# Kernel tuning notes

Measured on AMD Instinct MI355X. Metric: run time of the kernel, lower is better.

The kernel has to match this reference:

```python
import jax, jax.numpy as jnp
import numpy as np

N = 100_000  # nodes
E = 1_600_000  # edges (before self-loops)
NEG_SLOPE = 0.2  # PyG GATConv default leaky_relu slope


def gat_layer(x, W, a_src, a_dst, b, src, dst, heads, out_ch, concat):
    # x: [N, Fin]; W: [Fin, heads*out_ch]; a_src/a_dst: [1, heads, out_ch]
    h = (x @ W).reshape(-1, heads, out_ch)            # [N, H, C]
    alpha_s = jnp.sum(h * a_src, axis=-1)             # [N, H]
    alpha_d = jnp.sum(h * a_dst, axis=-1)             # [N, H]
    e = jax.nn.leaky_relu(alpha_s[src] + alpha_d[dst], NEG_SLOPE)  # [E', H]
    # softmax over edges grouped by destination node (self-loops guarantee
    # every node has at least one incoming edge)
    m = jax.ops.segment_max(e, dst, num_segments=N)   # [N, H]
    p = jnp.exp(e - m[dst])                           # [E', H]
    s = jax.ops.segment_sum(p, dst, num_segments=N)   # [N, H]
    alpha = p / s[dst]                                # [E', H]
    out = jax.ops.segment_sum(alpha[:, :, None] * h[src], dst, num_segments=N)  # [N,H,C]
    out = out.reshape(-1, heads * out_ch) if concat else out.mean(axis=1)
    return out + b


def setup_inputs() -> dict:
    key = jax.random.key(0)
    ks = jax.random.split(key, 8)

    def glorot(k, shape):
        return (jax.random.normal(k, shape, jnp.float32) / np.sqrt(np.float32(shape[0]))).astype(jnp.float32)

    x = jax.random.normal(ks[0], (N, 512), jnp.float32)
    edge_index = jax.random.randint(ks[1], (2, E), 0, N, dtype=jnp.int64)
    W1 = glorot(ks[2], (512, 64))
    att_src1 = jax.random.normal(ks[3], (1, 8, 8), jnp.float32) * 0.1
    att_dst1 = jax.random.normal(ks[4], (1, 8, 8), jnp.float32) * 0.1
    b1 = jnp.zeros((64,), jnp.float32)
    W2 = glorot(ks[5], (64, 128))
    att_src2 = jax.random.normal(ks[6], (1, 1, 128), jnp.float32) * 0.1
    att_dst2 = jax.random.normal(ks[7], (1, 1, 128), jnp.float32) * 0.1
    b2 = jnp.zeros((128,), jnp.float32)
    return {"x": x, "edge_index": edge_index, "W1": W1, "att_src1": att_src1,
            "att_dst1": att_dst1, "b1": b1, "W2": W2, "att_src2": att_src2,
            "att_dst2": att_dst2, "b2": b2}


def reference(x, edge_index, W1, att_src1, att_dst1, b1, W2, att_src2, att_dst2, b2):
    # PyG GATConv adds self-loops by default
    loop = jnp.arange(N, dtype=edge_index.dtype)
    src = jnp.concatenate([edge_index[0], loop])
    dst = jnp.concatenate([edge_index[1], loop])
    h = gat_layer(x, W1, att_src1, att_dst1, b1, src, dst, heads=8, out_ch=8, concat=True)
    h = jax.nn.elu(h)
    z = gat_layer(h, W2, att_src2, att_dst2, b2, src, dst, heads=1, out_ch=128, concat=False)
    return z
```

## Files before the change

kernel.cpp:

```cpp
#include <hip/hip_runtime.h>
#include <math.h>

#define NNODES 100000

__device__ __forceinline__ float lrelu(float v) { return v > 0.f ? v : 0.2f * v; }

#define SWZ(row) ((((row) & 3) ^ (((row) >> 3) & 7)) << 2)

__global__ __launch_bounds__(128) void gemm1_k(const float* __restrict__ x,
                                               const float* __restrict__ W,
                                               float* __restrict__ h1, int Nn) {
    __shared__ float xs[128][64];
    __shared__ float ws[64][64];
    int r0 = blockIdx.x * 128;
    int t = threadIdx.x;
    int ty = t >> 3, tx = t & 7;
    float acc0[8][4] = {};
    float acc1[8][4] = {};
    for (int kb = 0; kb < 512; kb += 64) {
        for (int l = t; l < 2048; l += 128) {
            int row = l >> 4;
            int c4 = (l & 15) << 2;
            int gr = r0 + row;
            float4 v = make_float4(0.f, 0.f, 0.f, 0.f);
            if (gr < Nn) v = *reinterpret_cast<const float4*>(&x[(size_t)gr * 512 + kb + c4]);
            *reinterpret_cast<float4*>(&xs[row][c4 ^ SWZ(row)]) = v;
        }
        for (int l = t; l < 1024; l += 128) {
            int row = l >> 4;
            int c4 = (l & 15) << 2;
            *reinterpret_cast<float4*>(&ws[row][c4]) =
                *reinterpret_cast<const float4*>(&W[(size_t)(kb + row) * 64 + c4]);
        }
        __syncthreads();
#pragma unroll 1
        for (int k0 = 0; k0 < 64; k0 += 4) {
            float4 av[8];
#pragma unroll
            for (int i = 0; i < 8; ++i) {
                int row = ty * 8 + i;
                av[i] = *reinterpret_cast<const float4*>(&xs[row][k0 ^ SWZ(row)]);
            }
            float4 b0[4], b1[4];
#pragma unroll
            for (int kk = 0; kk < 4; ++kk) {
                b0[kk] = *reinterpret_cast<const float4*>(&ws[k0 + kk][tx * 4]);
                b1[kk] = *reinterpret_cast<const float4*>(&ws[k0 + kk][32 + tx * 4]);
            }
#pragma unroll
            for (int kk = 0; kk < 4; ++kk) {
#pragma unroll
                for (int i = 0; i < 8; ++i) {
                    float a = (kk == 0) ? av[i].x : (kk == 1) ? av[i].y : (kk == 2) ? av[i].z : av[i].w;
                    acc0[i][0] += a * b0[kk].x; acc0[i][1] += a * b0[kk].y;
                    acc0[i][2] += a * b0[kk].z; acc0[i][3] += a * b0[kk].w;
                    acc1[i][0] += a * b1[kk].x; acc1[i][1] += a * b1[kk].y;
                    acc1[i][2] += a * b1[kk].z; acc1[i][3] += a * b1[kk].w;
                }
            }
        }
        __syncthreads();
    }
#pragma unroll
    for (int i = 0; i < 8; ++i) {
        int gr = r0 + ty * 8 + i;
        if (gr < Nn) {
            *reinterpret_cast<float4*>(&h1[(size_t)gr * 64 + tx * 4]) =
                make_float4(acc0[i][0], acc0[i][1], acc0[i][2], acc0[i][3]);
            *reinterpret_cast<float4*>(&h1[(size_t)gr * 64 + 32 + tx * 4]) =
                make_float4(acc1[i][0], acc1[i][1], acc1[i][2], acc1[i][3]);
        }
    }
}

__global__ __launch_bounds__(256) void gemm2_k(const float* __restrict__ xin,
                                               const float* __restrict__ W,
                                               float* __restrict__ h2, int Nn) {
    __shared__ float xs[128][64];
    __shared__ float ws[64][128];
    int r0 = blockIdx.x * 128;
    int t = threadIdx.x;
    int ty = t >> 4, tx = t & 15;
    for (int l = t; l < 2048; l += 256) {
        int row = l >> 4;
        int c4 = (l & 15) << 2;
        int gr = r0 + row;
        float4 v = make_float4(0.f, 0.f, 0.f, 0.f);
        if (gr < Nn) v = *reinterpret_cast<const float4*>(&xin[(size_t)gr * 64 + c4]);
        *reinterpret_cast<float4*>(&xs[row][c4 ^ SWZ(row)]) = v;
    }
    for (int l = t; l < 2048; l += 256) {
        int row = l >> 5;
        int c4 = (l & 31) << 2;
        *reinterpret_cast<float4*>(&ws[row][c4]) =
            *reinterpret_cast<const float4*>(&W[(size_t)row * 128 + c4]);
    }
    __syncthreads();
    float acc0[8][4] = {};
    float acc1[8][4] = {};
#pragma unroll 1
    for (int k0 = 0; k0 < 64; k0 += 4) {
        float4 av[8];
#pragma unroll
        for (int i = 0; i < 8; ++i) {
            int row = ty * 8 + i;
            av[i] = *reinterpret_cast<const float4*>(&xs[row][k0 ^ SWZ(row)]);
        }
        float4 b0[4], b1[4];
#pragma unroll
        for (int kk = 0; kk < 4; ++kk) {
            b0[kk] = *reinterpret_cast<const float4*>(&ws[k0 + kk][tx * 4]);
            b1[kk] = *reinterpret_cast<const float4*>(&ws[k0 + kk][64 + tx * 4]);
        }
#pragma unroll
        for (int kk = 0; kk < 4; ++kk) {
#pragma unroll
            for (int i = 0; i < 8; ++i) {
                float a = (kk == 0) ? av[i].x : (kk == 1) ? av[i].y : (kk == 2) ? av[i].z : av[i].w;
                acc0[i][0] += a * b0[kk].x; acc0[i][1] += a * b0[kk].y;
                acc0[i][2] += a * b0[kk].z; acc0[i][3] += a * b0[kk].w;
                acc1[i][0] += a * b1[kk].x; acc1[i][1] += a * b1[kk].y;
                acc1[i][2] += a * b1[kk].z; acc1[i][3] += a * b1[kk].w;
            }
        }
    }
#pragma unroll
    for (int i = 0; i < 8; ++i) {
        int gr = r0 + ty * 8 + i;
        if (gr < Nn) {
            *reinterpret_cast<float4*>(&h2[(size_t)gr * 128 + tx * 4]) =
                make_float4(acc0[i][0], acc0[i][1], acc0[i][2], acc0[i][3]);
            *reinterpret_cast<float4*>(&h2[(size_t)gr * 128 + 64 + tx * 4]) =
                make_float4(acc1[i][0], acc1[i][1], acc1[i][2], acc1[i][3]);
        }
    }
}

__global__ __launch_bounds__(256) void attn1_k(const float* __restrict__ h1,
                                               const float* __restrict__ asrc,
                                               const float* __restrict__ adst,
                                               float* __restrict__ as1,
                                               float* __restrict__ ad1, int Nn) {
    int t = blockIdx.x * 256 + threadIdx.x;
    int n = t >> 3, h = t & 7;
    if (n >= Nn) return;
    const float* hp = h1 + (size_t)n * 64 + h * 8;
    float s = 0.f, d = 0.f;
#pragma unroll
    for (int c = 0; c < 8; ++c) {
        float v = hp[c];
        s += v * asrc[h * 8 + c];
        d += v * adst[h * 8 + c];
    }
    as1[(size_t)n * 8 + h] = s;
    ad1[(size_t)n * 8 + h] = d;
}

__global__ __launch_bounds__(256) void attn2_k(const float* __restrict__ h2,
                                               const float* __restrict__ asrc,
                                               const float* __restrict__ adst,
                                               float* __restrict__ as2,
                                               float* __restrict__ ad2, int Nn) {
    int wid = threadIdx.x >> 6, lane = threadIdx.x & 63;
    int n = blockIdx.x * 4 + wid;
    if (n >= Nn) return;
    float v0 = h2[(size_t)n * 128 + lane];
    float v1 = h2[(size_t)n * 128 + 64 + lane];
    float s = v0 * asrc[lane] + v1 * asrc[64 + lane];
    float d = v0 * adst[lane] + v1 * adst[64 + lane];
#pragma unroll
    for (int off = 32; off >= 1; off >>= 1) {
        s += __shfl_xor(s, off);
        d += __shfl_xor(d, off);
    }
    if (lane == 0) { as2[n] = s; ad2[n] = d; }
}

__global__ __launch_bounds__(256) void hist_k(const int* __restrict__ ei, int E, int Etot,
                                              int* __restrict__ indeg) {
    int e = blockIdx.x * 256 + threadIdx.x;
    if (e >= Etot) return;
    int d = (e < E) ? ei[E + e] : (e - E);
    atomicAdd(&indeg[d], 1);
}

__global__ __launch_bounds__(256) void scanA_k(const int* __restrict__ indeg,
                                               int* __restrict__ indptr,
                                               int* __restrict__ bsums, int Nn) {
    __shared__ int sd[256];
    int t = threadIdx.x;
    int i0 = blockIdx.x * 2048 + t * 8;
    int v[8], ex[8];
    int run = 0;
#pragma unroll
    for (int j = 0; j < 8; ++j) {
        int i = i0 + j;
        v[j] = (i < Nn) ? indeg[i] : 0;
        ex[j] = run;
        run += v[j];
    }
    sd[t] = run;
    __syncthreads();
    for (int off = 1; off < 256; off <<= 1) {
        int a = (t >= off) ? sd[t - off] : 0;
        __syncthreads();
        sd[t] += a;
        __syncthreads();
    }
    int texc = sd[t] - run;
#pragma unroll
    for (int j = 0; j < 8; ++j) {
        int i = i0 + j;
        if (i < Nn) indptr[i] = texc + ex[j];
    }
    if (t == 0) bsums[blockIdx.x] = sd[255];
}

__global__ void scanB_k(int* __restrict__ bsums, int nb) {
    if (threadIdx.x == 0 && blockIdx.x == 0) {
        int run = 0;
        for (int b = 0; b < nb; ++b) {
            int x = bsums[b];
            bsums[b] = run;
            run += x;
        }
    }
}

__global__ __launch_bounds__(256) void scanC_k(int* __restrict__ indptr,
                                               const int* __restrict__ bsums,
                                               int* __restrict__ cursor, int Nn, int Etot) {
    int t = threadIdx.x;
    int b = blockIdx.x;
    int base = bsums[b];
    int i0 = b * 2048 + t * 8;
#pragma unroll
    for (int j = 0; j < 8; ++j) {
        int i = i0 + j;
        if (i < Nn) {
            int val = indptr[i] + base;
            indptr[i] = val;
            cursor[i] = val;
        }
    }
    if (b == 0 && t == 0) indptr[Nn] = Etot;
}

__global__ __launch_bounds__(256) void fill_k(const int* __restrict__ ei, int E, int Etot,
                                              int* __restrict__ cursor, int* __restrict__ col) {
    int e = blockIdx.x * 256 + threadIdx.x;
    if (e >= Etot) return;
    int s, d;
    if (e < E) { s = ei[e]; d = ei[E + e]; }
    else { s = e - E; d = e - E; }
    int pos = atomicAdd(&cursor[d], 1);
    col[pos] = s;
}

__global__ __launch_bounds__(256) void agg1_k(const float* __restrict__ h1,
                                              const float* __restrict__ as1,
                                              const float* __restrict__ ad1,
                                              const int* __restrict__ indptr,
                                              const int* __restrict__ col,
                                              const float* __restrict__ b1,
                                              float* __restrict__ h1a, int Nn) {
    int wid = threadIdx.x >> 6, lane = threadIdx.x & 63;
    int n = blockIdx.x * 4 + wid;
    if (n >= Nn) return;
    int beg = indptr[n], end = indptr[n + 1];
    int h = lane & 7, eo = lane >> 3;
    float adn = ad1[(size_t)n * 8 + h];
    float ss = 0.f;
    for (int i = beg + eo; i < end; i += 8) {
        int s = col[i];
        ss += __expf(lrelu(as1[(size_t)s * 8 + h] + adn));
    }
    ss += __shfl_xor(ss, 8);
    ss += __shfl_xor(ss, 16);
    ss += __shfl_xor(ss, 32);
    int hb = lane >> 3;
    float sb = __shfl(ss, hb);
    float ab = __shfl(adn, hb);
    float inv = 1.f / sb;
    const float* __restrict__ h1l = h1 + lane;
    float acc0 = 0.f, acc1 = 0.f, acc2 = 0.f, acc3 = 0.f;
    float acc4 = 0.f, acc5 = 0.f, acc6 = 0.f, acc7 = 0.f;
    int i = beg;
    for (; i + 8 <= end; i += 8) {
        int s0 = col[i], s1 = col[i + 1], s2 = col[i + 2], s3 = col[i + 3];
        int s4 = col[i + 4], s5 = col[i + 5], s6 = col[i + 6], s7 = col[i + 7];
        float w0 = __expf(lrelu(as1[(size_t)s0 * 8 + hb] + ab));
        float w1 = __expf(lrelu(as1[(size_t)s1 * 8 + hb] + ab));
        float w2 = __expf(lrelu(as1[(size_t)s2 * 8 + hb] + ab));
        float w3 = __expf(lrelu(as1[(size_t)s3 * 8 + hb] + ab));
        float w4 = __expf(lrelu(as1[(size_t)s4 * 8 + hb] + ab));
        float w5 = __expf(lrelu(as1[(size_t)s5 * 8 + hb] + ab));
        float w6 = __expf(lrelu(as1[(size_t)s6 * 8 + hb] + ab));
        float w7 = __expf(lrelu(as1[(size_t)s7 * 8 + hb] + ab));
        acc0 += w0 * h1l[(size_t)s0 * 64];
        acc1 += w1 * h1l[(size_t)s1 * 64];
        acc2 += w2 * h1l[(size_t)s2 * 64];
        acc3 += w3 * h1l[(size_t)s3 * 64];
        acc4 += w4 * h1l[(size_t)s4 * 64];
        acc5 += w5 * h1l[(size_t)s5 * 64];
        acc6 += w6 * h1l[(size_t)s6 * 64];
        acc7 += w7 * h1l[(size_t)s7 * 64];
    }
    for (; i < end; ++i) {
        int s = col[i];
        acc0 += __expf(lrelu(as1[(size_t)s * 8 + hb] + ab)) * h1l[(size_t)s * 64];
    }
    float o = (((acc0 + acc1) + (acc2 + acc3)) + ((acc4 + acc5) + (acc6 + acc7))) * inv + b1[lane];
    h1a[(size_t)n * 64 + lane] = o > 0.f ? o : expm1f(o);
}

__global__ __launch_bounds__(256) void agg2_k(const float* __restrict__ h2,
                                              const float* __restrict__ as2,
                                              const float* __restrict__ ad2,
                                              const int* __restrict__ indptr,
                                              const int* __restrict__ col,
                                              const float* __restrict__ b2,
                                              float* __restrict__ out, int Nn) {
    int wid = threadIdx.x >> 6, lane = threadIdx.x & 63;
    int n = blockIdx.x * 4 + wid;
    if (n >= Nn) return;
    int beg = indptr[n], end = indptr[n + 1];
    float adn = ad2[n];
    float ss = 0.f;
    for (int i = beg + lane; i < end; i += 64) {
        ss += __expf(lrelu(as2[col[i]] + adn));
    }
#pragma unroll
    for (int off = 32; off >= 1; off >>= 1) ss += __shfl_xor(ss, off);
    float inv = 1.f / ss;
    const float* __restrict__ h2l = h2 + lane;
    float a00 = 0.f, a01 = 0.f, a02 = 0.f, a03 = 0.f;
    float a04 = 0.f, a05 = 0.f, a06 = 0.f, a07 = 0.f;
    float a10 = 0.f, a11 = 0.f, a12 = 0.f, a13 = 0.f;
    float a14 = 0.f, a15 = 0.f, a16 = 0.f, a17 = 0.f;
    int i = beg;
    for (; i + 8 <= end; i += 8) {
        int s0 = col[i], s1 = col[i + 1], s2 = col[i + 2], s3 = col[i + 3];
        int s4 = col[i + 4], s5 = col[i + 5], s6 = col[i + 6], s7 = col[i + 7];
        float w0 = __expf(lrelu(as2[s0] + adn));
        float w1 = __expf(lrelu(as2[s1] + adn));
        float w2 = __expf(lrelu(as2[s2] + adn));
        float w3 = __expf(lrelu(as2[s3] + adn));
        float w4 = __expf(lrelu(as2[s4] + adn));
        float w5 = __expf(lrelu(as2[s5] + adn));
        float w6 = __expf(lrelu(as2[s6] + adn));
        float w7 = __expf(lrelu(as2[s7] + adn));
        a00 += w0 * h2l[(size_t)s0 * 128]; a10 += w0 * h2l[(size_t)s0 * 128 + 64];
        a01 += w1 * h2l[(size_t)s1 * 128]; a11 += w1 * h2l[(size_t)s1 * 128 + 64];
        a02 += w2 * h2l[(size_t)s2 * 128]; a12 += w2 * h2l[(size_t)s2 * 128 + 64];
        a03 += w3 * h2l[(size_t)s3 * 128]; a13 += w3 * h2l[(size_t)s3 * 128 + 64];
        a04 += w4 * h2l[(size_t)s4 * 128]; a14 += w4 * h2l[(size_t)s4 * 128 + 64];
        a05 += w5 * h2l[(size_t)s5 * 128]; a15 += w5 * h2l[(size_t)s5 * 128 + 64];
        a06 += w6 * h2l[(size_t)s6 * 128]; a16 += w6 * h2l[(size_t)s6 * 128 + 64];
        a07 += w7 * h2l[(size_t)s7 * 128]; a17 += w7 * h2l[(size_t)s7 * 128 + 64];
    }
    for (; i < end; ++i) {
        int s = col[i];
        float w = __expf(lrelu(as2[s] + adn));
        a00 += w * h2l[(size_t)s * 128];
        a10 += w * h2l[(size_t)s * 128 + 64];
    }
    float r0 = ((a00 + a01) + (a02 + a03)) + ((a04 + a05) + (a06 + a07));
    float r1 = ((a10 + a11) + (a12 + a13)) + ((a14 + a15) + (a16 + a17));
    out[(size_t)n * 128 + lane] = r0 * inv + b2[lane];
    out[(size_t)n * 128 + 64 + lane] = r1 * inv + b2[64 + lane];
}

extern "C" void kernel_launch(void* const* d_in, const int* in_sizes, int n_in,
                              void* d_out, int out_size, void* d_ws, size_t ws_size,
                              hipStream_t stream) {
    const float* x = (const float*)d_in[0];
    const int* ei = (const int*)d_in[1];
    const float* W1 = (const float*)d_in[2];
    const float* asrc1 = (const float*)d_in[3];
    const float* adst1 = (const float*)d_in[4];
    const float* b1 = (const float*)d_in[5];
    const float* W2 = (const float*)d_in[6];
    const float* asrc2 = (const float*)d_in[7];
    const float* adst2 = (const float*)d_in[8];
    const float* b2 = (const float*)d_in[9];
    float* out = (float*)d_out;

    const int Nn = NNODES;
    const int E = in_sizes[1] / 2;
    const int Etot = E + Nn;

    char* w = (char*)d_ws;
    auto alloc = [&](size_t bytes) {
        char* p = w;
        w += (bytes + 255) & ~(size_t)255;
        return p;
    };
    float* h1 = (float*)alloc((size_t)Nn * 64 * 4);
    float* h1a = (float*)alloc((size_t)Nn * 64 * 4);
    float* h2 = (float*)alloc((size_t)Nn * 128 * 4);
    float* as1 = (float*)alloc((size_t)Nn * 8 * 4);
    float* ad1 = (float*)alloc((size_t)Nn * 8 * 4);
    float* as2 = (float*)alloc((size_t)Nn * 4);
    float* ad2 = (float*)alloc((size_t)Nn * 4);
    int* indeg = (int*)alloc((size_t)(Nn + 1) * 4);
    int* indptr = (int*)alloc((size_t)(Nn + 1) * 4);
    int* cursor = (int*)alloc((size_t)Nn * 4);
    int* bsums = (int*)alloc(4096);
    int* col = (int*)alloc((size_t)Etot * 4);

    const int NBLK = (Nn + 2047) / 2048;

    hipMemsetAsync(indeg, 0, (size_t)Nn * 4, stream);
    gemm1_k<<<(Nn + 127) / 128, 128, 0, stream>>>(x, W1, h1, Nn);
    attn1_k<<<(Nn * 8 + 255) / 256, 256, 0, stream>>>(h1, asrc1, adst1, as1, ad1, Nn);
    hist_k<<<(Etot + 255) / 256, 256, 0, stream>>>(ei, E, Etot, indeg);
    scanA_k<<<NBLK, 256, 0, stream>>>(indeg, indptr, bsums, Nn);
    scanB_k<<<1, 64, 0, stream>>>(bsums, NBLK);
    scanC_k<<<NBLK, 256, 0, stream>>>(indptr, bsums, cursor, Nn, Etot);
    fill_k<<<(Etot + 255) / 256, 256, 0, stream>>>(ei, E, Etot, cursor, col);
    agg1_k<<<(Nn + 3) / 4, 256, 0, stream>>>(h1, as1, ad1, indptr, col, b1, h1a, Nn);
    gemm2_k<<<(Nn + 127) / 128, 256, 0, stream>>>(h1a, W2, h2, Nn);
    attn2_k<<<(Nn + 3) / 4, 256, 0, stream>>>(h2, asrc2, adst2, as2, ad2, Nn);
    agg2_k<<<(Nn + 3) / 4, 256, 0, stream>>>(h2, as2, ad2, indptr, col, b2, out, Nn);
}
```

Before: 1.010 ms.

## Prefetch next K-tile into registers in gemm1 and enlarge block to 256 rows

After: 883.0 us. -12.6%, faster.

```diff
diff --git a/kernel.cpp b/kernel.cpp
--- a/kernel.cpp
+++ b/kernel.cpp
@@ -7,56 +7,101 @@
 
 #define SWZ(row) ((((row) & 3) ^ (((row) >> 3) & 7)) << 2)
 
-__global__ __launch_bounds__(128) void gemm1_k(const float* __restrict__ x,
+__global__ __launch_bounds__(256) void gemm1_k(const float* __restrict__ x,
                                                const float* __restrict__ W,
                                                float* __restrict__ h1, int Nn) {
-    __shared__ float xs[128][64];
+    __shared__ float xs[256][64];
     __shared__ float ws[64][64];
-    int r0 = blockIdx.x * 128;
+    int r0 = blockIdx.x * 256;
     int t = threadIdx.x;
     int ty = t >> 3, tx = t & 7;
-    float acc0[8][4] = {};
-    float acc1[8][4] = {};
+    float4 xr[16], wr[4];
+    float acc[8][8] = {};
+
+#pragma unroll
+    for (int n = 0; n < 16; ++n) {
+        int l = t + n * 256;
+        int row = l >> 4, c4 = (l & 15) << 2;
+        int gr = r0 + row;
+        xr[n] = make_float4(0.f, 0.f, 0.f, 0.f);
+        if (gr < Nn) xr[n] = *reinterpret_cast<const float4*>(&x[(size_t)gr * 512 + c4]);
+    }
+#pragma unroll
+    for (int n = 0; n < 4; ++n) {
+        int l = t + n * 256;
+        int row = l >> 4, c4 = (l & 15) << 2;
+        wr[n] = *reinterpret_cast<const float4*>(&W[(size_t)row * 64 + c4]);
+    }
+#pragma unroll
+    for (int n = 0; n < 16; ++n) {
+        int l = t + n * 256;
+        int row = l >> 4, c4 = (l & 15) << 2;
+        *reinterpret_cast<float4*>(&xs[row][c4 ^ SWZ(row)]) = xr[n];
+    }
+#pragma unroll
+    for (int n = 0; n < 4; ++n) {
+        int l = t + n * 256;
+        int row = l >> 4, c4 = (l & 15) << 2;
+        *reinterpret_cast<float4*>(&ws[row][c4]) = wr[n];
+    }
+    __syncthreads();
+
     for (int kb = 0; kb < 512; kb += 64) {
-        for (int l = t; l < 2048; l += 128) {
-            int row = l >> 4;
-            int c4 = (l & 15) << 2;
-            int gr = r0 + row;
-            float4 v = make_float4(0.f, 0.f, 0.f, 0.f);
-            if (gr < Nn) v = *reinterpret_cast<const float4*>(&x[(size_t)gr * 512 + kb + c4]);
-            *reinterpret_cast<float4*>(&xs[row][c4 ^ SWZ(row)]) = v;
-        }
-        for (int l = t; l < 1024; l += 128) {
-            int row = l >> 4;
-            int c4 = (l & 15) << 2;
-            *reinterpret_cast<float4*>(&ws[row][c4]) =
-                *reinterpret_cast<const float4*>(&W[(size_t)(kb + row) * 64 + c4]);
-        }
-        __syncthreads();
+        bool more = (kb + 64 < 512);
+        if (more) {
+#pragma unroll
+            for (int n = 0; n < 16; ++n) {
+                int l = t + n * 256;
+                int row = l >> 4, c4 = (l & 15) << 2;
+                int gr = r0 + row;
+                xr[n] = make_float4(0.f, 0.f, 0.f, 0.f);
+                if (gr < Nn) xr[n] = *reinterpret_cast<const float4*>(&x[(size_t)gr * 512 + kb + 64 + c4]);
+            }
+#pragma unroll
+            for (int n = 0; n < 4; ++n) {
+                int l = t + n * 256;
+                int row = l >> 4, c4 = (l & 15) << 2;
+                wr[n] = *reinterpret_cast<const float4*>(&W[(size_t)(kb + 64 + row) * 64 + c4]);
+            }
+        }
 #pragma unroll 1
         for (int k0 = 0; k0 < 64; k0 += 4) {
-            float4 av[8];
+            float4 av[8], ba[4], bb[4];
 #pragma unroll
             for (int i = 0; i < 8; ++i) {
                 int row = ty * 8 + i;
                 av[i] = *reinterpret_cast<const float4*>(&xs[row][k0 ^ SWZ(row)]);
             }
-            float4 b0[4], b1[4];
 #pragma unroll
             for (int kk = 0; kk < 4; ++kk) {
-                b0[kk] = *reinterpret_cast<const float4*>(&ws[k0 + kk][tx * 4]);
-                b1[kk] = *reinterpret_cast<const float4*>(&ws[k0 + kk][32 + tx * 4]);
+                ba[kk] = *reinterpret_cast<const float4*>(&ws[k0 + kk][tx * 8]);
+                bb[kk] = *reinterpret_cast<const float4*>(&ws[k0 + kk][tx * 8 + 4]);
             }
 #pragma unroll
             for (int kk = 0; kk < 4; ++kk) {
 #pragma unroll
                 for (int i = 0; i < 8; ++i) {
                     float a = (kk == 0) ? av[i].x : (kk == 1) ? av[i].y : (kk == 2) ? av[i].z : av[i].w;
-                    acc0[i][0] += a * b0[kk].x; acc0[i][1] += a * b0[kk].y;
-                    acc0[i][2] += a * b0[kk].z; acc0[i][3] += a * b0[kk].w;
-                    acc1[i][0] += a * b1[kk].x; acc1[i][1] += a * b1[kk].y;
-                    acc1[i][2] += a * b1[kk].z; acc1[i][3] += a * b1[kk].w;
+                    acc[i][0] += a * ba[kk].x; acc[i][1] += a * ba[kk].y;
+                    acc[i][2] += a * ba[kk].z; acc[i][3] += a * ba[kk].w;
+                    acc[i][4] += a * bb[kk].x; acc[i][5] += a * bb[kk].y;
+                    acc[i][6] += a * bb[kk].z; acc[i][7] += a * bb[kk].w;
                 }
+            }
+        }
+        __syncthreads();
+        if (more) {
+#pragma unroll
+            for (int n = 0; n < 16; ++n) {
+                int l = t + n * 256;
+                int row = l >> 4, c4 = (l & 15) << 2;
+                *reinterpret_cast<float4*>(&xs[row][c4 ^ SWZ(row)]) = xr[n];
+            }
+#pragma unroll
+            for (int n = 0; n < 4; ++n) {
+                int l = t + n * 256;
+                int row = l >> 4, c4 = (l & 15) << 2;
+                *reinterpret_cast<float4*>(&ws[row][c4]) = wr[n];
             }
         }
         __syncthreads();
@@ -65,10 +110,10 @@
     for (int i = 0; i < 8; ++i) {
         int gr = r0 + ty * 8 + i;
         if (gr < Nn) {
-            *reinterpret_cast<float4*>(&h1[(size_t)gr * 64 + tx * 4]) =
-                make_float4(acc0[i][0], acc0[i][1], acc0[i][2], acc0[i][3]);
-            *reinterpret_cast<float4*>(&h1[(size_t)gr * 64 + 32 + tx * 4]) =
-                make_float4(acc1[i][0], acc1[i][1], acc1[i][2], acc1[i][3]);
+            *reinterpret_cast<float4*>(&h1[(size_t)gr * 64 + tx * 8]) =
+                make_float4(acc[i][0], acc[i][1], acc[i][2], acc[i][3]);
+            *reinterpret_cast<float4*>(&h1[(size_t)gr * 64 + tx * 8 + 4]) =
+                make_float4(acc[i][4], acc[i][5], acc[i][6], acc[i][7]);
         }
     }
 }
@@ -82,16 +127,14 @@
     int t = threadIdx.x;
     int ty = t >> 4, tx = t & 15;
     for (int l = t; l < 2048; l += 256) {
-        int row = l >> 4;
-        int c4 = (l & 15) << 2;
+        int row = l >> 4, c4 = (l & 15) << 2;
         int gr = r0 + row;
         float4 v = make_float4(0.f, 0.f, 0.f, 0.f);
         if (gr < Nn) v = *reinterpret_cast<const float4*>(&xin[(size_t)gr * 64 + c4]);
         *reinterpret_cast<float4*>(&xs[row][c4 ^ SWZ(row)]) = v;
     }
     for (int l = t; l < 2048; l += 256) {
-        int row = l >> 5;
-        int c4 = (l & 31) << 2;
+        int row = l >> 5, c4 = (l & 31) << 2;
         *reinterpret_cast<float4*>(&ws[row][c4]) =
             *reinterpret_cast<const float4*>(&W[(size_t)row * 128 + c4]);
     }
@@ -100,27 +143,26 @@
     float acc1[8][4] = {};
 #pragma unroll 1
     for (int k0 = 0; k0 < 64; k0 += 4) {
-        float4 av[8];
+        float4 av[8], ba[4], bb[4];
 #pragma unroll
         for (int i = 0; i < 8; ++i) {
             int row = ty * 8 + i;
             av[i] = *reinterpret_cast<const float4*>(&xs[row][k0 ^ SWZ(row)]);
         }
-        float4 b0[4], b1[4];
 #pragma unroll
         for (int kk = 0; kk < 4; ++kk) {
-            b0[kk] = *reinterpret_cast<const float4*>(&ws[k0 + kk][tx * 4]);
-            b1[kk] = *reinterpret_cast<const float4*>(&ws[k0 + kk][64 + tx * 4]);
+            ba[kk] = *reinterpret_cast<const float4*>(&ws[k0 + kk][tx * 4]);
+            bb[kk] = *reinterpret_cast<const float4*>(&ws[k0 + kk][64 + tx * 4]);
         }
 #pragma unroll
         for (int kk = 0; kk < 4; ++kk) {
 #pragma unroll
             for (int i = 0; i < 8; ++i) {
                 float a = (kk == 0) ? av[i].x : (kk == 1) ? av[i].y : (kk == 2) ? av[i].z : av[i].w;
-                acc0[i][0] += a * b0[kk].x; acc0[i][1] += a * b0[kk].y;
-                acc0[i][2] += a * b0[kk].z; acc0[i][3] += a * b0[kk].w;
-                acc1[i][0] += a * b1[kk].x; acc1[i][1] += a * b1[kk].y;
-                acc1[i][2] += a * b1[kk].z; acc1[i][3] += a * b1[kk].w;
+                acc0[i][0] += a * ba[kk].x; acc0[i][1] += a * ba[kk].y;
+                acc0[i][2] += a * ba[kk].z; acc0[i][3] += a * ba[kk].w;
+                acc1[i][0] += a * bb[kk].x; acc1[i][1] += a * bb[kk].y;
+                acc1[i][2] += a * bb[kk].z; acc1[i][3] += a * bb[kk].w;
             }
         }
     }
@@ -412,7 +454,7 @@
     const int NBLK = (Nn + 2047) / 2048;
 
     hipMemsetAsync(indeg, 0, (size_t)Nn * 4, stream);
-    gemm1_k<<<(Nn + 127) / 128, 128, 0, stream>>>(x, W1, h1, Nn);
+    gemm1_k<<<(Nn + 255) / 256, 256, 0, stream>>>(x, W1, h1, Nn);
     attn1_k<<<(Nn * 8 + 255) / 256, 256, 0, stream>>>(h1, asrc1, adst1, as1, ad1, Nn);
     hist_k<<<(Etot + 255) / 256, 256, 0, stream>>>(ei, E, Etot, indeg);
     scanA_k<<<NBLK, 256, 0, stream>>>(indeg, indptr, bsums, Nn);
```

## Read GEMM weights directly from global memory and retile threads in both GEMMs

Applied to the files above, without the earlier changes.

New measurement: 944.5 us. -6.5%, faster.

```diff
diff --git a/kernel.cpp b/kernel.cpp
--- a/kernel.cpp
+++ b/kernel.cpp
@@ -7,68 +7,59 @@
 
 #define SWZ(row) ((((row) & 3) ^ (((row) >> 3) & 7)) << 2)
 
-__global__ __launch_bounds__(128) void gemm1_k(const float* __restrict__ x,
+__global__ __launch_bounds__(256) void gemm1_k(const float* __restrict__ x,
                                                const float* __restrict__ W,
                                                float* __restrict__ h1, int Nn) {
     __shared__ float xs[128][64];
-    __shared__ float ws[64][64];
     int r0 = blockIdx.x * 128;
     int t = threadIdx.x;
     int ty = t >> 3, tx = t & 7;
-    float acc0[8][4] = {};
-    float acc1[8][4] = {};
+    int srow = t >> 4;
+    int sc4 = (t & 15) << 2;
+    float acc[4][8] = {};
     for (int kb = 0; kb < 512; kb += 64) {
-        for (int l = t; l < 2048; l += 128) {
-            int row = l >> 4;
-            int c4 = (l & 15) << 2;
+        __syncthreads();
+#pragma unroll
+        for (int n = 0; n < 8; ++n) {
+            int row = srow + n * 16;
             int gr = r0 + row;
-            float4 v = make_float4(0.f, 0.f, 0.f, 0.f);
-            if (gr < Nn) v = *reinterpret_cast<const float4*>(&x[(size_t)gr * 512 + kb + c4]);
-            *reinterpret_cast<float4*>(&xs[row][c4 ^ SWZ(row)]) = v;
-        }
-        for (int l = t; l < 1024; l += 128) {
-            int row = l >> 4;
-            int c4 = (l & 15) << 2;
-            *reinterpret_cast<float4*>(&ws[row][c4]) =
-                *reinterpret_cast<const float4*>(&W[(size_t)(kb + row) * 64 + c4]);
+            int cr = gr < Nn ? gr : Nn - 1;
+            float4 v = *reinterpret_cast<const float4*>(&x[(size_t)cr * 512 + kb + sc4]);
+            *reinterpret_cast<float4*>(&xs[row][sc4 ^ SWZ(row)]) = v;
         }
         __syncthreads();
+        const float* Wb = W + (size_t)kb * 64;
 #pragma unroll 1
         for (int k0 = 0; k0 < 64; k0 += 4) {
-            float4 av[8];
-#pragma unroll
-            for (int i = 0; i < 8; ++i) {
-                int row = ty * 8 + i;
+            float4 av[4];
+#pragma unroll
+            for (int i = 0; i < 4; ++i) {
+                int row = ty * 4 + i;
                 av[i] = *reinterpret_cast<const float4*>(&xs[row][k0 ^ SWZ(row)]);
             }
-            float4 b0[4], b1[4];
 #pragma unroll
             for (int kk = 0; kk < 4; ++kk) {
-                b0[kk] = *reinterpret_cast<const float4*>(&ws[k0 + kk][tx * 4]);
-                b1[kk] = *reinterpret_cast<const float4*>(&ws[k0 + kk][32 + tx * 4]);
-            }
-#pragma unroll
-            for (int kk = 0; kk < 4; ++kk) {
-#pragma unroll
-                for (int i = 0; i < 8; ++i) {
+                float4 b0 = *reinterpret_cast<const float4*>(&Wb[(k0 + kk) * 64 + tx * 8]);
+                float4 b1 = *reinterpret_cast<const float4*>(&Wb[(k0 + kk) * 64 + tx * 8 + 4]);
+#pragma unroll
+                for (int i = 0; i < 4; ++i) {
                     float a = (kk == 0) ? av[i].x : (kk == 1) ? av[i].y : (kk == 2) ? av[i].z : av[i].w;
-                    acc0[i][0] += a * b0[kk].x; acc0[i][1] += a * b0[kk].y;
-                    acc0[i][2] += a * b0[kk].z; acc0[i][3] += a * b0[kk].w;
-                    acc1[i][0] += a * b1[kk].x; acc1[i][1] += a * b1[kk].y;
-                    acc1[i][2] += a * b1[kk].z; acc1[i][3] += a * b1[kk].w;
+                    acc[i][0] += a * b0.x; acc[i][1] += a * b0.y;
+                    acc[i][2] += a * b0.z; acc[i][3] += a * b0.w;
+                    acc[i][4] += a * b1.x; acc[i][5] += a * b1.y;
+                    acc[i][6] += a * b1.z; acc[i][7] += a * b1.w;
                 }
             }
         }
-        __syncthreads();
-    }
-#pragma unroll
-    for (int i = 0; i < 8; ++i) {
-        int gr = r0 + ty * 8 + i;
+    }
+#pragma unroll
+    for (int i = 0; i < 4; ++i) {
+        int gr = r0 + ty * 4 + i;
         if (gr < Nn) {
-            *reinterpret_cast<float4*>(&h1[(size_t)gr * 64 + tx * 4]) =
-                make_float4(acc0[i][0], acc0[i][1], acc0[i][2], acc0[i][3]);
-            *reinterpret_cast<float4*>(&h1[(size_t)gr * 64 + 32 + tx * 4]) =
-                make_float4(acc1[i][0], acc1[i][1], acc1[i][2], acc1[i][3]);
+            *reinterpret_cast<float4*>(&h1[(size_t)gr * 64 + tx * 8]) =
+                make_float4(acc[i][0], acc[i][1], acc[i][2], acc[i][3]);
+            *reinterpret_cast<float4*>(&h1[(size_t)gr * 64 + tx * 8 + 4]) =
+                make_float4(acc[i][4], acc[i][5], acc[i][6], acc[i][7]);
         }
     }
 }
@@ -77,61 +68,59 @@
                                                const float* __restrict__ W,
                                                float* __restrict__ h2, int Nn) {
     __shared__ float xs[128][64];
-    __shared__ float ws[64][128];
     int r0 = blockIdx.x * 128;
     int t = threadIdx.x;
-    int ty = t >> 4, tx = t & 15;
-    for (int l = t; l < 2048; l += 256) {
-        int row = l >> 4;
-        int c4 = (l & 15) << 2;
+    int ty = t >> 3, tx = t & 7;
+    int srow = t >> 4;
+    int sc4 = (t & 15) << 2;
+#pragma unroll
+    for (int n = 0; n < 8; ++n) {
+        int row = srow + n * 16;
         int gr = r0 + row;
-        float4 v = make_float4(0.f, 0.f, 0.f, 0.f);
-        if (gr < Nn) v = *reinterpret_cast<const float4*>(&xin[(size_t)gr * 64 + c4]);
-        *reinterpret_cast<float4*>(&xs[row][c4 ^ SWZ(row)]) = v;
-    }
-    for (int l = t; l < 2048; l += 256) {
-        int row = l >> 5;
-        int c4 = (l & 31) << 2;
-        *reinterpret_cast<float4*>(&ws[row][c4]) =
-            *reinterpret_cast<const float4*>(&W[(size_t)row * 128 + c4]);
+        int cr = gr < Nn ? gr : Nn - 1;
+        float4 v = *reinterpret_cast<const float4*>(&xin[(size_t)cr * 64 + sc4]);
+        *reinterpret_cast<float4*>(&xs[row][sc4 ^ SWZ(row)]) = v;
     }
     __syncthreads();
-    float acc0[8][4] = {};
-    float acc1[8][4] = {};
+    float acc[4][16] = {};
 #pragma unroll 1
     for (int k0 = 0; k0 < 64; k0 += 4) {
-        float4 av[8];
-#pragma unroll
-        for (int i = 0; i < 8; ++i) {
-            int row = ty * 8 + i;
+        float4 av[4];
+#pragma unroll
+        for (int i = 0; i < 4; ++i) {
+            int row = ty * 4 + i;
             av[i] = *reinterpret_cast<const float4*>(&xs[row][k0 ^ SWZ(row)]);
         }
-        float4 b0[4], b1[4];
 #pragma unroll
         for (int kk = 0; kk < 4; ++kk) {
-            b0[kk] = *reinterpret_cast<const float4*>(&ws[k0 + kk][tx * 4]);
-            b1[kk] = *reinterpret_cast<const float4*>(&ws[k0 + kk][64 + tx * 4]);
-        }
-#pragma unroll
-        for (int kk = 0; kk < 4; ++kk) {
-#pragma unroll
-            for (int i = 0; i < 8; ++i) {
+            const float* wr = &W[(size_t)(k0 + kk) * 128 + tx * 16];
+            float4 b0 = *reinterpret_cast<const float4*>(wr);
+            float4 b1 = *reinterpret_cast<const float4*>(wr + 4);
+            float4 b2 = *reinterpret_cast<const float4*>(wr + 8);
+            float4 b3 = *reinterpret_cast<const float4*>(wr + 12);
+#pragma unroll
+            for (int i = 0; i < 4; ++i) {
                 float a = (kk == 0) ? av[i].x : (kk == 1) ? av[i].y : (kk == 2) ? av[i].z : av[i].w;
-                acc0[i][0] += a * b0[kk].x; acc0[i][1] += a * b0[kk].y;
-                acc0[i][2] += a * b0[kk].z; acc0[i][3] += a * b0[kk].w;
-                acc1[i][0] += a * b1[kk].x; acc1[i][1] += a * b1[kk].y;
-                acc1[i][2] += a * b1[kk].z; acc1[i][3] += a * b1[kk].w;
+                acc[i][0] += a * b0.x;  acc[i][1] += a * b0.y;
+                acc[i][2] += a * b0.z;  acc[i][3] += a * b0.w;
+                acc[i][4] += a * b1.x;  acc[i][5] += a * b1.y;
+                acc[i][6] += a * b1.z;  acc[i][7] += a * b1.w;
+                acc[i][8] += a * b2.x;  acc[i][9] += a * b2.y;
+                acc[i][10] += a * b2.z; acc[i][11] += a * b2.w;
+                acc[i][12] += a * b3.x; acc[i][13] += a * b3.y;
+                acc[i][14] += a * b3.z; acc[i][15] += a * b3.w;
             }
         }
     }
 #pragma unroll
-    for (int i = 0; i < 8; ++i) {
-        int gr = r0 + ty * 8 + i;
+    for (int i = 0; i < 4; ++i) {
+        int gr = r0 + ty * 4 + i;
         if (gr < Nn) {
-            *reinterpret_cast<float4*>(&h2[(size_t)gr * 128 + tx * 4]) =
-                make_float4(acc0[i][0], acc0[i][1], acc0[i][2], acc0[i][3]);
-            *reinterpret_cast<float4*>(&h2[(size_t)gr * 128 + 64 + tx * 4]) =
-                make_float4(acc1[i][0], acc1[i][1], acc1[i][2], acc1[i][3]);
+            float* op = &h2[(size_t)gr * 128 + tx * 16];
+            *reinterpret_cast<float4*>(op) = make_float4(acc[i][0], acc[i][1], acc[i][2], acc[i][3]);
+            *reinterpret_cast<float4*>(op + 4) = make_float4(acc[i][4], acc[i][5], acc[i][6], acc[i][7]);
+            *reinterpret_cast<float4*>(op + 8) = make_float4(acc[i][8], acc[i][9], acc[i][10], acc[i][11]);
+            *reinterpret_cast<float4*>(op + 12) = make_float4(acc[i][12], acc[i][13], acc[i][14], acc[i][15]);
         }
     }
 }
@@ -412,7 +401,7 @@
     const int NBLK = (Nn + 2047) / 2048;
 
     hipMemsetAsync(indeg, 0, (size_t)Nn * 4, stream);
-    gemm1_k<<<(Nn + 127) / 128, 128, 0, stream>>>(x, W1, h1, Nn);
+    gemm1_k<<<(Nn + 127) / 128, 256, 0, stream>>>(x, W1, h1, Nn);
     attn1_k<<<(Nn * 8 + 255) / 256, 256, 0, stream>>>(h1, asrc1, adst1, as1, ad1, Nn);
     hist_k<<<(Etot + 255) / 256, 256, 0, stream>>>(ei, E, Etot, indeg);
     scanA_k<<<NBLK, 256, 0, stream>>>(indeg, indptr, bsums, Nn);
```
